# Kernel tuning notes

Measured on AMD Instinct MI355X. Metric: run time of the kernel, lower is better.

Reference implementation:

```python
import jax, jax.numpy as jnp
import numpy as np

# ---- hash-grid config (from module source) ----
L = 16          # n_levels
F = 2           # n_features_per_level
T = 1 << 19     # hashmap size
BASE = 16
SCALE = 1.3819
RES = [int(np.floor(BASE * SCALE ** l)) for l in range(L)]
DENSE = [(r + 1) ** 3 <= T for r in RES]   # levels 0-4 dense, rest hashed
PRIMES = np.array([1, 2654435761, 805459861], dtype=np.uint32)
OFFS = np.array([[i, j, k] for k in (0, 1) for j in (0, 1) for i in (0, 1)], dtype=np.float32)  # [8,3]
OFFS_U = OFFS.astype(np.uint32)


def hash_grid_encode(xyz, table):
    # xyz: [N,3] in [0,1); table: [L,T,F]
    feats = []
    for l in range(L):
        res = RES[l]
        pos = xyz * res                      # [N,3]
        p0f = jnp.floor(pos)
        w = pos - p0f                        # trilinear weights, [N,3]
        p0 = p0f.astype(jnp.uint32)          # [N,3]
        corner = p0[:, None, :] + OFFS_U[None]            # [N,8,3] uint32
        if DENSE[l]:
            s = np.uint32(res + 1)
            idx = corner[..., 0] + corner[..., 1] * s + corner[..., 2] * (s * s)
        else:
            idx = (corner[..., 0] * PRIMES[0]) ^ (corner[..., 1] * PRIMES[1]) ^ (corner[..., 2] * PRIMES[2])
            idx = idx % np.uint32(T)
        # corner weights: prod_d (offs ? w : 1-w)  -> [N,8]
        wts = jnp.prod(jnp.where(OFFS[None].astype(bool), w[:, None, :], 1.0 - w[:, None, :]), axis=-1)
        f = table[l][idx]                    # gather: [N,8,F]
        feats.append(jnp.sum(f * wts[..., None], axis=1))  # [N,F]
    return jnp.concatenate(feats, axis=-1)   # [N, L*F=32]


def sh_deg4(d):
    # d in [-1,1]^3; returns [N,16] real SH basis (tcnn ordering/constants)
    x, y, z = d[:, 0], d[:, 1], d[:, 2]
    x2, y2, z2 = x * x, y * y, z * z
    xy, yz, xz = x * y, y * z, x * z
    return jnp.stack([
        jnp.full_like(x, 0.28209479177387814),
        -0.48860251190291987 * y,
        0.48860251190291987 * z,
        -0.48860251190291987 * x,
        1.0925484305920792 * xy,
        -1.0925484305920792 * yz,
        0.94617469575755997 * z2 - 0.31539156525251999,
        -1.0925484305920792 * xz,
        0.54627421529603959 * (x2 - y2),
        0.59004358992664352 * y * (-3.0 * x2 + y2),
        2.8906114426405538 * xy * z,
        0.45704579946446572 * y * (1.0 - 5.0 * z2),
        0.3731763325901154 * z * (5.0 * z2 - 3.0),
        0.45704579946446572 * x * (1.0 - 5.0 * z2),
        1.4453057213202769 * z * (x2 - y2),
        0.59004358992664352 * x * (-x2 + 3.0 * y2),
    ], axis=-1)


def setup_inputs() -> dict:
    key = jax.random.key(0)
    ks = jax.random.split(key, 8)
    N = 2 ** 21
    xyz = jax.random.uniform(ks[0], (N, 3), dtype=jnp.float32)
    dir = jax.random.uniform(ks[1], (N, 3), dtype=jnp.float32)
    # hash table init per tcnn: uniform in [-1e-4, 1e-4]
    hash_table = jax.random.uniform(ks[2], (L, T, F), dtype=jnp.float32, minval=-1e-4, maxval=1e-4)
    def he(k, fan_in, shape):
        return jax.random.normal(k, shape, dtype=jnp.float32) * np.sqrt(2.0 / fan_in)
    w_sigma1 = he(ks[3], 32, (32, 64))
    w_sigma2 = he(ks[4], 64, (64, 17))   # 1 + geo_feat_dim(16)
    w_rgb1 = he(ks[5], 32, (32, 64))     # 16 (SH) + 16 (geo)
    w_rgb2 = he(ks[6], 64, (64, 64))
    w_rgb3 = he(ks[7], 64, (64, 3))
    return {"xyz": xyz, "dir": dir, "hash_table": hash_table,
            "w_sigma1": w_sigma1, "w_sigma2": w_sigma2,
            "w_rgb1": w_rgb1, "w_rgb2": w_rgb2, "w_rgb3": w_rgb3}


def reference(xyz, dir, hash_table, w_sigma1, w_sigma2, w_rgb1, w_rgb2, w_rgb3):
    xyz_flat = xyz.reshape(-1, 3)
    dir_flat = dir.reshape(-1, 3)
    enc = hash_grid_encode(xyz_flat, hash_table)                 # [N,32]
    h = jax.nn.relu(enc @ w_sigma1)
    geometry = h @ w_sigma2                                       # [N,17]
    sigma, geo_feat = geometry[..., :1], geometry[..., 1:]
    dir_enc = sh_deg4(dir_flat * 2.0 - 1.0)                       # [N,16]
    rgb_in = jnp.concatenate([dir_enc, geo_feat], axis=-1)        # [N,32]
    h = jax.nn.relu(rgb_in @ w_rgb1)
    h = jax.nn.relu(h @ w_rgb2)
    rgb = h @ w_rgb3                                              # [N,3]
    rgb_unflat = rgb.reshape(xyz.shape)
    sigma_unflat = sigma.reshape(xyz.shape[:-1] + (1,))
    return jax.nn.sigmoid(rgb_unflat), jax.nn.relu(sigma_unflat)
```

## Files before the change

### kernel.cpp

```cpp
#include <hip/hip_runtime.h>
#include <hip/hip_bf16.h>
#include <cmath>

#define TBL (1 << 19)

__device__ __forceinline__ float relu_f(float x) { return fmaxf(x, 0.0f); }

__device__ __forceinline__ unsigned short f2bf(float x) {
    union { float f; unsigned u; } v; v.f = x;
    const unsigned r = v.u + 0x7FFFu + ((v.u >> 16) & 1u);
    return (unsigned short)(r >> 16);
}

typedef __attribute__((ext_vector_type(8))) short short8;
typedef __attribute__((ext_vector_type(4))) float floatx4;

__device__ __forceinline__ int sperm(int k) {
    return ((k >> 5) << 5) | (((k >> 2) & 3) << 3) | (((k >> 4) & 1) << 2) | (k & 3);
}

#define RES_LIST {16, 22, 30, 42, 58, 80, 111, 153, 212, 294, 406, 561, 775, 1072, 1481, 2047}

__global__ __launch_bounds__(256, 8)
void encode_sched(const float* __restrict__ xyz,
                  const float* __restrict__ table,
                  unsigned* __restrict__ ws_enc,
                  int n)
{
    constexpr unsigned RES[16] = RES_LIST;
    constexpr int LEVORD[16] = {5, 0, 6, 1, 7, 2, 8, 3, 9, 4, 10, 11, 12, 13, 14, 15};

    const int xcd      = (int)(blockIdx.x & 7u);
    const unsigned g   = blockIdx.x >> 3;
    const unsigned upb = (unsigned)(n >> 11);
    const int unit     = (int)(g / upb);
    const int slot     = (int)(g % upb);
    const int level    = LEVORD[unit & 15];
    const int i        = xcd * (n >> 3) + slot * 256 + (int)threadIdx.x;
    if (i >= n) return;

    const float px_ = __builtin_nontemporal_load(xyz + 3 * (size_t)i + 0);
    const float py_ = __builtin_nontemporal_load(xyz + 3 * (size_t)i + 1);
    const float pz_ = __builtin_nontemporal_load(xyz + 3 * (size_t)i + 2);

    const unsigned res = RES[level];
    const float fr = (float)res;
    const float posx = px_ * fr, posy = py_ * fr, posz = pz_ * fr;
    const float fx = floorf(posx), fy = floorf(posy), fz = floorf(posz);
    const float wx = posx - fx, wy = posy - fy, wz = posz - fz;
    const unsigned x0 = (unsigned)fx, y0 = (unsigned)fy, z0 = (unsigned)fz;
    const float* tb = table + (size_t)level * (TBL * 2);

    float a0 = 0.0f, a1 = 0.0f;
    const float wx1 = wx, wx0 = 1.0f - wx;

    if (level < 5) {
        const unsigned s = res + 1u;
        const unsigned s2 = s * s;
        const unsigned base = x0 + y0 * s + z0 * s2;
#pragma unroll
        for (int c = 0; c < 4; ++c) {
            const unsigned dy = c & 1, dz = c >> 1;
            const unsigned idx = base + dy * s + dz * s2;
            const float wyz = (dy ? wy : 1.0f - wy) * (dz ? wz : 1.0f - wz);
            const float w0 = wyz * wx0, w1 = wyz * wx1;
            float e0x, e0y, e1x, e1y;
            if (!(idx & 1u)) {
                const float4 f = *reinterpret_cast<const float4*>(tb + 2u * idx);
                e0x = f.x; e0y = f.y; e1x = f.z; e1y = f.w;
            } else {
                const float2 f0 = *reinterpret_cast<const float2*>(tb + 2u * idx);
                const float2 f1 = *reinterpret_cast<const float2*>(tb + 2u * idx + 2u);
                e0x = f0.x; e0y = f0.y; e1x = f1.x; e1y = f1.y;
            }
            a0 = fmaf(e0x, w0, fmaf(e1x, w1, a0));
            a1 = fmaf(e0y, w0, fmaf(e1y, w1, a1));
        }
    } else {
#pragma unroll
        for (int c = 0; c < 4; ++c) {
            const unsigned dy = c & 1, dz = c >> 1;
            const unsigned hh = (y0 + dy) * 2654435761u ^ (z0 + dz) * 805459861u;
            const float wyz = (dy ? wy : 1.0f - wy) * (dz ? wz : 1.0f - wz);
            const float w0 = wyz * wx0, w1 = wyz * wx1;
            const unsigned i0 = (x0 ^ hh) & (unsigned)(TBL - 1);
            if (!(x0 & 1u)) {
                const float4 f = *reinterpret_cast<const float4*>(tb + 2u * (i0 & ~1u));
                const bool hi = (i0 & 1u) != 0u;
                const float e0x = hi ? f.z : f.x, e0y = hi ? f.w : f.y;
                const float e1x = hi ? f.x : f.z, e1y = hi ? f.y : f.w;
                a0 = fmaf(e0x, w0, fmaf(e1x, w1, a0));
                a1 = fmaf(e0y, w0, fmaf(e1y, w1, a1));
            } else {
                const unsigned i1 = ((x0 + 1u) ^ hh) & (unsigned)(TBL - 1);
                const float2 f0 = *reinterpret_cast<const float2*>(tb + 2u * i0);
                const float2 f1 = *reinterpret_cast<const float2*>(tb + 2u * i1);
                a0 = fmaf(f0.x, w0, fmaf(f1.x, w1, a0));
                a1 = fmaf(f0.y, w0, fmaf(f1.y, w1, a1));
            }
        }
    }

    const unsigned pack = (unsigned)f2bf(a0) | ((unsigned)f2bf(a1) << 16);
    __builtin_nontemporal_store(pack, ws_enc + ((size_t)level * n + i));
}

__global__ __launch_bounds__(256)
void mlp_mfma(const unsigned* __restrict__ ws_enc,
              const float* __restrict__ dirv,
              const float* __restrict__ ws1,
              const float* __restrict__ ws2,
              const float* __restrict__ wr1,
              const float* __restrict__ wr2,
              const float* __restrict__ wr3,
              float* __restrict__ out,
              int n)
{
    __shared__ alignas(16) unsigned short s_w[12032];
    __shared__ alignas(8)  unsigned short s_geo[4][16 * 20];

    const int tid = threadIdx.x;

    for (int e = tid; e < 12032; e += 256) s_w[e] = 0;
    __syncthreads();
    for (int e = tid; e < 2048; e += 256) { const int k = e >> 6, j = e & 63; s_w[0    + j * 40 + k] = f2bf(ws1[e]); }
    for (int e = tid; e < 1088; e += 256) { const int k = e / 17, j = e % 17; s_w[2560 + j * 72 + sperm(k)] = f2bf(ws2[e]); }
    for (int e = tid; e < 2048; e += 256) { const int k = e >> 6, j = e & 63; s_w[4864 + j * 40 + k] = f2bf(wr1[e]); }
    for (int e = tid; e < 4096; e += 256) { const int k = e >> 6, j = e & 63; s_w[7424 + j * 72 + sperm(k)] = f2bf(wr2[e]); }
    __syncthreads();

    const int wave = tid >> 6;
    const int lane = tid & 63;
    const int q    = lane >> 4;
    const int mr   = lane & 15;
    unsigned short* gb = s_geo[wave];
    const int base = blockIdx.x * 1024 + wave * 256;
    if (base >= n) return;

    float w3v[4][3];
#pragma unroll
    for (int t = 0; t < 4; ++t)
#pragma unroll
        for (int c = 0; c < 3; ++c)
            w3v[t][c] = wr3[(t * 16 + mr) * 3 + c];

    const int pt0 = base + mr;
    unsigned e0 = ws_enc[(size_t)(q * 4 + 0) * n + pt0];
    unsigned e1 = ws_enc[(size_t)(q * 4 + 1) * n + pt0];
    unsigned e2 = ws_enc[(size_t)(q * 4 + 2) * n + pt0];
    unsigned e3 = ws_enc[(size_t)(q * 4 + 3) * n + pt0];
    float dv0 = dirv[3 * (size_t)pt0 + 0];
    float dv1 = dirv[3 * (size_t)pt0 + 1];
    float dv2 = dirv[3 * (size_t)pt0 + 2];

    union U8 { unsigned u[4]; short8 s; };

#pragma unroll 1
    for (int it = 0; it < 16; ++it) {
        const int pb = base + it * 16;

        unsigned f0 = 0, f1 = 0, f2 = 0, f3 = 0;
        float c0 = 0.f, c1 = 0.f, c2 = 0.f;
        if (it < 15) {
            const int ptn = pt0 + (it + 1) * 16;
            f0 = ws_enc[(size_t)(q * 4 + 0) * n + ptn];
            f1 = ws_enc[(size_t)(q * 4 + 1) * n + ptn];
            f2 = ws_enc[(size_t)(q * 4 + 2) * n + ptn];
            f3 = ws_enc[(size_t)(q * 4 + 3) * n + ptn];
            c0 = dirv[3 * (size_t)ptn + 0];
            c1 = dirv[3 * (size_t)ptn + 1];
            c2 = dirv[3 * (size_t)ptn + 2];
        }

        U8 be; be.u[0] = e0; be.u[1] = e1; be.u[2] = e2; be.u[3] = e3;
        const short8 benc = be.s;

        floatx4 h4[4];
#pragma unroll
        for (int t = 0; t < 4; ++t) {
            const short8 a = *reinterpret_cast<const short8*>(s_w + 0 + (t * 16 + mr) * 40 + q * 8);
            floatx4 acc = {0.f, 0.f, 0.f, 0.f};
            h4[t] = __builtin_amdgcn_mfma_f32_16x16x32_bf16(a, benc, acc, 0, 0, 0);
        }

        short8 A0, A1;
#pragma unroll
        for (int j = 0; j < 4; ++j) {
            A0[j]     = (short)f2bf(fmaxf(h4[0][j], 0.f));
            A0[4 + j] = (short)f2bf(fmaxf(h4[1][j], 0.f));
            A1[j]     = (short)f2bf(fmaxf(h4[2][j], 0.f));
            A1[4 + j] = (short)f2bf(fmaxf(h4[3][j], 0.f));
        }

        floatx4 g0acc = {0.f, 0.f, 0.f, 0.f};
        floatx4 g1acc = {0.f, 0.f, 0.f, 0.f};
        {
            const short8 b00 = *reinterpret_cast<const short8*>(s_w + 2560 + mr * 72 + 0  + q * 8);
            const short8 b01 = *reinterpret_cast<const short8*>(s_w + 2560 + mr * 72 + 32 + q * 8);
            g0acc = __builtin_amdgcn_mfma_f32_16x16x32_bf16(A0, b00, g0acc, 0, 0, 0);
            g0acc = __builtin_amdgcn_mfma_f32_16x16x32_bf16(A1, b01, g0acc, 0, 0, 0);
            const short8 b10 = *reinterpret_cast<const short8*>(s_w + 2560 + (16 + mr) * 72 + 0  + q * 8);
            const short8 b11 = *reinterpret_cast<const short8*>(s_w + 2560 + (16 + mr) * 72 + 32 + q * 8);
            g1acc = __builtin_amdgcn_mfma_f32_16x16x32_bf16(A0, b10, g1acc, 0, 0, 0);
            g1acc = __builtin_amdgcn_mfma_f32_16x16x32_bf16(A1, b11, g1acc, 0, 0, 0);
        }

        if (mr == 0) {
#pragma unroll
            for (int r = 0; r < 4; ++r)
                out[3 * (size_t)n + (size_t)(pb + q * 4 + r)] = fmaxf(g0acc[r], 0.f);
        }

        if (mr != 0) {
#pragma unroll
            for (int r = 0; r < 4; ++r)
                gb[(q * 4 + r) * 20 + (mr - 1)] = f2bf(g0acc[r]);
        } else {
#pragma unroll
            for (int r = 0; r < 4; ++r)
                gb[(q * 4 + r) * 20 + 15] = f2bf(g1acc[r]);
        }
        __builtin_amdgcn_wave_barrier();

        const float dx = dv0 * 2.0f - 1.0f;
        const float dy = dv1 * 2.0f - 1.0f;
        const float dz = dv2 * 2.0f - 1.0f;
        const float x2 = dx * dx, y2 = dy * dy, z2 = dz * dz;
        const float xy = dx * dy, yz = dy * dz, xz = dx * dz;
        const float s0  = 0.28209479177387814f;
        const float s1  = -0.48860251190291987f * dy;
        const float s2  = 0.48860251190291987f * dz;
        const float s3  = -0.48860251190291987f * dx;
        const float s4  = 1.0925484305920792f * xy;
        const float s5  = -1.0925484305920792f * yz;
        const float s6  = 0.94617469575756f * z2 - 0.31539156525252f;
        const float s7  = -1.0925484305920792f * xz;
        const float s8  = 0.5462742152960396f * (x2 - y2);
        const float s9  = 0.5900435899266435f * dy * (-3.0f * x2 + y2);
        const float s10 = 2.890611442640554f * xy * dz;
        const float s11 = 0.4570457994644657f * dy * (1.0f - 5.0f * z2);
        const float s12 = 0.3731763325901154f * dz * (5.0f * z2 - 3.0f);
        const float s13 = 0.4570457994644657f * dx * (1.0f - 5.0f * z2);
        const float s14 = 1.445305721320277f * dz * (x2 - y2);
        const float s15 = 0.5900435899266435f * dx * (-x2 + 3.0f * y2);

        const bool qh = (q & 1) != 0;
        const float u0 = qh ? s8  : s0;
        const float u1 = qh ? s9  : s1;
        const float u2 = qh ? s10 : s2;
        const float u3 = qh ? s11 : s3;
        const float u4 = qh ? s12 : s4;
        const float u5 = qh ? s13 : s5;
        const float u6 = qh ? s14 : s6;
        const float u7 = qh ? s15 : s7;
        const unsigned shw0 = (unsigned)f2bf(u0) | ((unsigned)f2bf(u1) << 16);
        const unsigned shw1 = (unsigned)f2bf(u2) | ((unsigned)f2bf(u3) << 16);
        const unsigned shw2 = (unsigned)f2bf(u4) | ((unsigned)f2bf(u5) << 16);
        const unsigned shw3 = (unsigned)f2bf(u6) | ((unsigned)f2bf(u7) << 16);

        const int sb = (q & 1) * 8;
        const unsigned* gp = reinterpret_cast<const unsigned*>(gb + mr * 20 + sb);
        U8 br;
        br.u[0] = (q < 2) ? shw0 : gp[0];
        br.u[1] = (q < 2) ? shw1 : gp[1];
        br.u[2] = (q < 2) ? shw2 : gp[2];
        br.u[3] = (q < 2) ? shw3 : gp[3];
        const short8 brgb = br.s;

        floatx4 gg[4];
#pragma unroll
        for (int t = 0; t < 4; ++t) {
            const short8 a = *reinterpret_cast<const short8*>(s_w + 4864 + (t * 16 + mr) * 40 + q * 8);
            floatx4 acc = {0.f, 0.f, 0.f, 0.f};
            gg[t] = __builtin_amdgcn_mfma_f32_16x16x32_bf16(a, brgb, acc, 0, 0, 0);
        }

        short8 Ag0, Ag1;
#pragma unroll
        for (int j = 0; j < 4; ++j) {
            Ag0[j]     = (short)f2bf(fmaxf(gg[0][j], 0.f));
            Ag0[4 + j] = (short)f2bf(fmaxf(gg[1][j], 0.f));
            Ag1[j]     = (short)f2bf(fmaxf(gg[2][j], 0.f));
            Ag1[4 + j] = (short)f2bf(fmaxf(gg[3][j], 0.f));
        }

        floatx4 g2[4];
#pragma unroll
        for (int t = 0; t < 4; ++t) {
            const short8 b0 = *reinterpret_cast<const short8*>(s_w + 7424 + (t * 16 + mr) * 72 + 0  + q * 8);
            const short8 b1 = *reinterpret_cast<const short8*>(s_w + 7424 + (t * 16 + mr) * 72 + 32 + q * 8);
            floatx4 acc = {0.f, 0.f, 0.f, 0.f};
            acc = __builtin_amdgcn_mfma_f32_16x16x32_bf16(Ag0, b0, acc, 0, 0, 0);
            acc = __builtin_amdgcn_mfma_f32_16x16x32_bf16(Ag1, b1, acc, 0, 0, 0);
            g2[t] = acc;
        }

        float part[3][4];
#pragma unroll
        for (int c = 0; c < 3; ++c)
#pragma unroll
            for (int r = 0; r < 4; ++r) part[c][r] = 0.f;
#pragma unroll
        for (int t = 0; t < 4; ++t) {
#pragma unroll
            for (int r = 0; r < 4; ++r) {
                const float v = fmaxf(g2[t][r], 0.f);
#pragma unroll
                for (int c = 0; c < 3; ++c) part[c][r] = fmaf(v, w3v[t][c], part[c][r]);
            }
        }
#pragma unroll
        for (int m = 1; m < 16; m <<= 1) {
#pragma unroll
            for (int c = 0; c < 3; ++c)
#pragma unroll
                for (int r = 0; r < 4; ++r)
                    part[c][r] += __shfl_xor(part[c][r], m);
        }
        if (mr == 0) {
#pragma unroll
            for (int r = 0; r < 4; ++r)
                out[3 * (size_t)(pb + q * 4 + r) + 0] = 1.0f / (1.0f + __expf(-part[0][r]));
        } else if (mr == 1) {
#pragma unroll
            for (int r = 0; r < 4; ++r)
                out[3 * (size_t)(pb + q * 4 + r) + 1] = 1.0f / (1.0f + __expf(-part[1][r]));
        } else if (mr == 2) {
#pragma unroll
            for (int r = 0; r < 4; ++r)
                out[3 * (size_t)(pb + q * 4 + r) + 2] = 1.0f / (1.0f + __expf(-part[2][r]));
        }
        __builtin_amdgcn_wave_barrier();

        e0 = f0; e1 = f1; e2 = f2; e3 = f3;
        dv0 = c0; dv1 = c1; dv2 = c2;
    }
}

__global__ __launch_bounds__(256, 4)
void nerf_fused(const float* __restrict__ xyz,
                const float* __restrict__ dirv,
                const float* __restrict__ table,
                const float* __restrict__ ws1,
                const float* __restrict__ ws2,
                const float* __restrict__ wr1,
                const float* __restrict__ wr2,
                const float* __restrict__ wr3,
                float* __restrict__ out,
                int n)
{
    constexpr unsigned RES[16] = RES_LIST;

    const int i = blockIdx.x * 256 + threadIdx.x;
    if (i >= n) return;

    const float px_ = xyz[3 * (size_t)i + 0];
    const float py_ = xyz[3 * (size_t)i + 1];
    const float pz_ = xyz[3 * (size_t)i + 2];

    float enc[32];
#pragma unroll
    for (int l = 0; l < 16; ++l) {
        const unsigned res = RES[l];
        const float fr = (float)res;
        const float posx = px_ * fr, posy = py_ * fr, posz = pz_ * fr;
        const float fx = floorf(posx), fy = floorf(posy), fz = floorf(posz);
        const float wx = posx - fx, wy = posy - fy, wz = posz - fz;
        const unsigned x0 = (unsigned)fx, y0 = (unsigned)fy, z0 = (unsigned)fz;
        const float* tb = table + (size_t)l * (TBL * 2);
        float a0 = 0.0f, a1 = 0.0f;
#pragma unroll
        for (int c = 0; c < 8; ++c) {
            const unsigned cx = x0 + (c & 1);
            const unsigned cy = y0 + ((c >> 1) & 1);
            const unsigned cz = z0 + ((c >> 2) & 1);
            unsigned idx;
            if (l < 5) {
                const unsigned s = res + 1u;
                idx = cx + cy * s + cz * (s * s);
            } else {
                idx = (cx * 1u) ^ (cy * 2654435761u) ^ (cz * 805459861u);
                idx &= (unsigned)(TBL - 1);
            }
            const float w = ((c & 1) ? wx : 1.0f - wx) *
                            ((c & 2) ? wy : 1.0f - wy) *
                            ((c & 4) ? wz : 1.0f - wz);
            const float2 f = *reinterpret_cast<const float2*>(tb + 2u * idx);
            a0 = fmaf(f.x, w, a0);
            a1 = fmaf(f.y, w, a1);
        }
        enc[2 * l + 0] = a0;
        enc[2 * l + 1] = a1;
    }

    float h[64];
#pragma unroll
    for (int j = 0; j < 64; ++j) h[j] = 0.0f;
#pragma unroll
    for (int k = 0; k < 32; ++k) {
        const float e = enc[k];
#pragma unroll
        for (int j = 0; j < 64; ++j) h[j] = fmaf(e, ws1[k * 64 + j], h[j]);
    }
#pragma unroll
    for (int j = 0; j < 64; ++j) h[j] = relu_f(h[j]);

    float geo[17];
#pragma unroll
    for (int j = 0; j < 17; ++j) geo[j] = 0.0f;
#pragma unroll
    for (int k = 0; k < 64; ++k) {
        const float e = h[k];
#pragma unroll
        for (int j = 0; j < 17; ++j) geo[j] = fmaf(e, ws2[k * 17 + j], geo[j]);
    }
    out[3 * (size_t)n + (size_t)i] = relu_f(geo[0]);

    const float dx = dirv[3 * (size_t)i + 0] * 2.0f - 1.0f;
    const float dy = dirv[3 * (size_t)i + 1] * 2.0f - 1.0f;
    const float dz = dirv[3 * (size_t)i + 2] * 2.0f - 1.0f;
    const float x2 = dx * dx, y2 = dy * dy, z2 = dz * dz;
    const float xy = dx * dy, yz = dy * dz, xz = dx * dz;

    float sh[16];
    sh[0]  = 0.28209479177387814f;
    sh[1]  = -0.48860251190291987f * dy;
    sh[2]  = 0.48860251190291987f * dz;
    sh[3]  = -0.48860251190291987f * dx;
    sh[4]  = 1.0925484305920792f * xy;
    sh[5]  = -1.0925484305920792f * yz;
    sh[6]  = 0.94617469575756f * z2 - 0.31539156525252f;
    sh[7]  = -1.0925484305920792f * xz;
    sh[8]  = 0.5462742152960396f * (x2 - y2);
    sh[9]  = 0.5900435899266435f * dy * (-3.0f * x2 + y2);
    sh[10] = 2.890611442640554f * xy * dz;
    sh[11] = 0.4570457994644657f * dy * (1.0f - 5.0f * z2);
    sh[12] = 0.3731763325901154f * dz * (5.0f * z2 - 3.0f);
    sh[13] = 0.4570457994644657f * dx * (1.0f - 5.0f * z2);
    sh[14] = 1.445305721320277f * dz * (x2 - y2);
    sh[15] = 0.5900435899266435f * dx * (-x2 + 3.0f * y2);

    float g[64];
#pragma unroll
    for (int j = 0; j < 64; ++j) g[j] = 0.0f;
#pragma unroll
    for (int k = 0; k < 16; ++k) {
        const float e = sh[k];
#pragma unroll
        for (int j = 0; j < 64; ++j) g[j] = fmaf(e, wr1[k * 64 + j], g[j]);
    }
#pragma unroll
    for (int k = 16; k < 32; ++k) {
        const float e = geo[k - 15];
#pragma unroll
        for (int j = 0; j < 64; ++j) g[j] = fmaf(e, wr1[k * 64 + j], g[j]);
    }
#pragma unroll
    for (int j = 0; j < 64; ++j) g[j] = relu_f(g[j]);

    float r0 = 0.0f, r1 = 0.0f, r2 = 0.0f;
#pragma unroll
    for (int half = 0; half < 2; ++half) {
        const int j0 = half * 32;
        float g2h[32];
#pragma unroll
        for (int j = 0; j < 32; ++j) g2h[j] = 0.0f;
#pragma unroll
        for (int k = 0; k < 64; ++k) {
            const float e = g[k];
#pragma unroll
            for (int j = 0; j < 32; ++j) g2h[j] = fmaf(e, wr2[k * 64 + j0 + j], g2h[j]);
        }
#pragma unroll
        for (int j = 0; j < 32; ++j) {
            const float e = relu_f(g2h[j]);
            r0 = fmaf(e, wr3[(j0 + j) * 3 + 0], r0);
            r1 = fmaf(e, wr3[(j0 + j) * 3 + 1], r1);
            r2 = fmaf(e, wr3[(j0 + j) * 3 + 2], r2);
        }
    }

    out[3 * (size_t)i + 0] = 1.0f / (1.0f + __expf(-r0));
    out[3 * (size_t)i + 1] = 1.0f / (1.0f + __expf(-r1));
    out[3 * (size_t)i + 2] = 1.0f / (1.0f + __expf(-r2));
}

extern "C" void kernel_launch(void* const* d_in, const int* in_sizes, int n_in,
                              void* d_out, int out_size, void* d_ws, size_t ws_size,
                              hipStream_t stream)
{
    const float* xyz   = (const float*)d_in[0];
    const float* dirv  = (const float*)d_in[1];
    const float* table = (const float*)d_in[2];
    const float* ws1   = (const float*)d_in[3];
    const float* ws2   = (const float*)d_in[4];
    const float* wr1   = (const float*)d_in[5];
    const float* wr2   = (const float*)d_in[6];
    const float* wr3   = (const float*)d_in[7];
    float* out = (float*)d_out;

    const int n = in_sizes[0] / 3;
    dim3 block(256);

    const size_t enc_bytes = (size_t)n * 16 * sizeof(unsigned);
    if (ws_size >= enc_bytes && n >= 2048 && (n & 2047) == 0) {
        unsigned* ws_enc = (unsigned*)d_ws;
        dim3 grid_enc(8u * 16u * (unsigned)(n >> 11));
        dim3 grid_mlp((unsigned)(n >> 10));
        hipLaunchKernelGGL(encode_sched, grid_enc, block, 0, stream,
                           xyz, table, ws_enc, n);
        hipLaunchKernelGGL(mlp_mfma, grid_mlp, block, 0, stream,
                           ws_enc, dirv, ws1, ws2, wr1, wr2, wr3, out, n);
    } else {
        dim3 grid_mlp((n + 255) / 256);
        hipLaunchKernelGGL(nerf_fused, grid_mlp, block, 0, stream,
                           xyz, dirv, table, ws1, ws2, wr1, wr2, wr3, out, n);
    }
}
```

Baseline: 953.4 us.

## Sort points into spatial buckets before hash-grid encoding for gather locality

Adds a counting sort of points into a 32^3 spatial grid (zero, histogram, single-block scan, atomic scatter) and runs the encoder on the sorted coordinates. The MLP reads directions and writes outputs through the resulting permutation. The goal is to make the hash-table gathers of neighbouring threads hit nearby or identical table entries, improving cache hit rates. The cost is four extra kernel launches, a serial single-block scan, atomic contention in the histogram, and scattered direction reads and output writes in the MLP.

```diff
diff --git a/kernel.cpp b/kernel.cpp
--- a/kernel.cpp
+++ b/kernel.cpp
@@ -3,6 +3,7 @@
 #include <cmath>
 
 #define TBL (1 << 19)
+#define NBUCKET 32768
 
 __device__ __forceinline__ float relu_f(float x) { return fmaxf(x, 0.0f); }
 
@@ -19,7 +20,73 @@
     return ((k >> 5) << 5) | (((k >> 2) & 3) << 3) | (((k >> 4) & 1) << 2) | (k & 3);
 }
 
+__device__ __forceinline__ unsigned bucket_of(float x, float y, float z) {
+    unsigned bx = (unsigned)(x * 32.0f); bx = bx > 31u ? 31u : bx;
+    unsigned by = (unsigned)(y * 32.0f); by = by > 31u ? 31u : by;
+    unsigned bz = (unsigned)(z * 32.0f); bz = bz > 31u ? 31u : bz;
+    return (bz << 10) | (by << 5) | bx;
+}
+
 #define RES_LIST {16, 22, 30, 42, 58, 80, 111, 153, 212, 294, 406, 561, 775, 1072, 1481, 2047}
+
+__global__ void zero_hist(unsigned* __restrict__ hist)
+{
+    const int i = blockIdx.x * 256 + threadIdx.x;
+    if (i < NBUCKET) hist[i] = 0u;
+}
+
+__global__ void hist_k(const float* __restrict__ xyz, unsigned* __restrict__ hist, int n)
+{
+    const int i = blockIdx.x * 256 + threadIdx.x;
+    if (i >= n) return;
+    const float x = xyz[3 * (size_t)i + 0];
+    const float y = xyz[3 * (size_t)i + 1];
+    const float z = xyz[3 * (size_t)i + 2];
+    atomicAdd(&hist[bucket_of(x, y, z)], 1u);
+}
+
+__global__ __launch_bounds__(1024)
+void scan_k(const unsigned* __restrict__ hist, unsigned* __restrict__ base)
+{
+    __shared__ unsigned buf[1024];
+    __shared__ unsigned carry;
+    const int t = threadIdx.x;
+    if (t == 0) carry = 0u;
+    __syncthreads();
+    for (int c = 0; c < NBUCKET / 1024; ++c) {
+        const unsigned x = hist[c * 1024 + t];
+        buf[t] = x;
+        __syncthreads();
+        for (int off = 1; off < 1024; off <<= 1) {
+            const unsigned v = (t >= off) ? buf[t - off] : 0u;
+            __syncthreads();
+            buf[t] += v;
+            __syncthreads();
+        }
+        base[c * 1024 + t] = carry + buf[t] - x;
+        __syncthreads();
+        if (t == 1023) carry += buf[1023];
+        __syncthreads();
+    }
+}
+
+__global__ void scatter_k(const float* __restrict__ xyz,
+                          unsigned* __restrict__ base,
+                          unsigned* __restrict__ perm,
+                          float* __restrict__ xyz_s,
+                          int n)
+{
+    const int i = blockIdx.x * 256 + threadIdx.x;
+    if (i >= n) return;
+    const float x = xyz[3 * (size_t)i + 0];
+    const float y = xyz[3 * (size_t)i + 1];
+    const float z = xyz[3 * (size_t)i + 2];
+    const unsigned pos = atomicAdd(&base[bucket_of(x, y, z)], 1u);
+    perm[pos] = (unsigned)i;
+    xyz_s[3 * (size_t)pos + 0] = x;
+    xyz_s[3 * (size_t)pos + 1] = y;
+    xyz_s[3 * (size_t)pos + 2] = z;
+}
 
 __global__ __launch_bounds__(256, 8)
 void encode_sched(const float* __restrict__ xyz,
@@ -108,6 +175,7 @@
 __global__ __launch_bounds__(256)
 void mlp_mfma(const unsigned* __restrict__ ws_enc,
               const float* __restrict__ dirv,
+              const unsigned* __restrict__ perm,
               const float* __restrict__ ws1,
               const float* __restrict__ ws2,
               const float* __restrict__ wr1,
@@ -149,9 +217,10 @@
     unsigned e1 = ws_enc[(size_t)(q * 4 + 1) * n + pt0];
     unsigned e2 = ws_enc[(size_t)(q * 4 + 2) * n + pt0];
     unsigned e3 = ws_enc[(size_t)(q * 4 + 3) * n + pt0];
-    float dv0 = dirv[3 * (size_t)pt0 + 0];
-    float dv1 = dirv[3 * (size_t)pt0 + 1];
-    float dv2 = dirv[3 * (size_t)pt0 + 2];
+    const unsigned o0 = perm[pt0];
+    float dv0 = dirv[3 * (size_t)o0 + 0];
+    float dv1 = dirv[3 * (size_t)o0 + 1];
+    float dv2 = dirv[3 * (size_t)o0 + 2];
 
     union U8 { unsigned u[4]; short8 s; };
 
@@ -167,9 +236,10 @@
             f1 = ws_enc[(size_t)(q * 4 + 1) * n + ptn];
             f2 = ws_enc[(size_t)(q * 4 + 2) * n + ptn];
             f3 = ws_enc[(size_t)(q * 4 + 3) * n + ptn];
-            c0 = dirv[3 * (size_t)ptn + 0];
-            c1 = dirv[3 * (size_t)ptn + 1];
-            c2 = dirv[3 * (size_t)ptn + 2];
+            const unsigned on = perm[ptn];
+            c0 = dirv[3 * (size_t)on + 0];
+            c1 = dirv[3 * (size_t)on + 1];
+            c2 = dirv[3 * (size_t)on + 2];
         }
 
         U8 be; be.u[0] = e0; be.u[1] = e1; be.u[2] = e2; be.u[3] = e3;
@@ -208,7 +278,7 @@
         if (mr == 0) {
 #pragma unroll
             for (int r = 0; r < 4; ++r)
-                out[3 * (size_t)n + (size_t)(pb + q * 4 + r)] = fmaxf(g0acc[r], 0.f);
+                out[3 * (size_t)n + (size_t)perm[pb + q * 4 + r]] = fmaxf(g0acc[r], 0.f);
         }
 
         if (mr != 0) {
@@ -320,15 +390,15 @@
         if (mr == 0) {
 #pragma unroll
             for (int r = 0; r < 4; ++r)
-                out[3 * (size_t)(pb + q * 4 + r) + 0] = 1.0f / (1.0f + __expf(-part[0][r]));
+                out[3 * (size_t)perm[pb + q * 4 + r] + 0] = 1.0f / (1.0f + __expf(-part[0][r]));
         } else if (mr == 1) {
 #pragma unroll
             for (int r = 0; r < 4; ++r)
-                out[3 * (size_t)(pb + q * 4 + r) + 1] = 1.0f / (1.0f + __expf(-part[1][r]));
+                out[3 * (size_t)perm[pb + q * 4 + r] + 1] = 1.0f / (1.0f + __expf(-part[1][r]));
         } else if (mr == 2) {
 #pragma unroll
             for (int r = 0; r < 4; ++r)
-                out[3 * (size_t)(pb + q * 4 + r) + 2] = 1.0f / (1.0f + __expf(-part[2][r]));
+                out[3 * (size_t)perm[pb + q * 4 + r] + 2] = 1.0f / (1.0f + __expf(-part[2][r]));
         }
         __builtin_amdgcn_wave_barrier();
 
@@ -502,15 +572,29 @@
     const int n = in_sizes[0] / 3;
     dim3 block(256);
 
-    const size_t enc_bytes = (size_t)n * 16 * sizeof(unsigned);
-    if (ws_size >= enc_bytes && n >= 2048 && (n & 2047) == 0) {
+    const size_t enc_w  = (size_t)n * 16;
+    const size_t xyzs_w = (size_t)n * 3;
+    const size_t perm_w = (size_t)n;
+    const size_t need_b = (enc_w + xyzs_w + perm_w + 2 * NBUCKET) * 4;
+    if (ws_size >= need_b && n >= 2048 && (n & 2047) == 0) {
         unsigned* ws_enc = (unsigned*)d_ws;
+        float*    xyz_s  = (float*)(ws_enc + enc_w);
+        unsigned* perm   = (unsigned*)(xyz_s + xyzs_w);
+        unsigned* hist   = perm + perm_w;
+        unsigned* bbase  = hist + NBUCKET;
+
+        const unsigned pblk = (unsigned)((n + 255) / 256);
+        hipLaunchKernelGGL(zero_hist, dim3(NBUCKET / 256), block, 0, stream, hist);
+        hipLaunchKernelGGL(hist_k,    dim3(pblk), block, 0, stream, xyz, hist, n);
+        hipLaunchKernelGGL(scan_k,    dim3(1), dim3(1024), 0, stream, hist, bbase);
+        hipLaunchKernelGGL(scatter_k, dim3(pblk), block, 0, stream, xyz, bbase, perm, xyz_s, n);
+
         dim3 grid_enc(8u * 16u * (unsigned)(n >> 11));
+        hipLaunchKernelGGL(encode_sched, grid_enc, block, 0, stream,
+                           xyz_s, table, ws_enc, n);
         dim3 grid_mlp((unsigned)(n >> 10));
-        hipLaunchKernelGGL(encode_sched, grid_enc, block, 0, stream,
-                           xyz, table, ws_enc, n);
         hipLaunchKernelGGL(mlp_mfma, grid_mlp, block, 0, stream,
-                           ws_enc, dirv, ws1, ws2, wr1, wr2, wr3, out, n);
+                           ws_enc, dirv, perm, ws1, ws2, wr1, wr2, wr3, out, n);
     } else {
         dim3 grid_mlp((n + 255) / 256);
         hipLaunchKernelGGL(nerf_fused, grid_mlp, block, 0, stream,
```

Result: slower. 1.112 ms (+16.7%).
